# Kernel tuning notes

Hardware: AMD Instinct MI355X
Metric: run time of the kernel (lower is better)

The kernel has to match this reference:

```python
import jax, jax.numpy as jnp
import numpy as np

N_NODES = 50000
N_EDGES = 640000
IN_CH = 128
OUT_CH = 128
HID = 2 * OUT_CH  # 256


def _glorot(key, shape):
    fan_in, fan_out = shape
    lim = np.sqrt(6.0 / (fan_in + fan_out)).astype(np.float32)
    return jax.random.uniform(key, shape, jnp.float32, -lim, lim)


def setup_inputs() -> dict:
    key = jax.random.key(0)
    ks = jax.random.split(key, 8)
    x = jax.random.normal(ks[0], (N_NODES, IN_CH), jnp.float32)
    edge_index = jax.random.randint(ks[1], (2, N_EDGES), 0, N_NODES, jnp.int64)
    # SAGEConv layer 1: lin_l (neighbor branch, with bias), lin_r (root branch, no bias)
    w1_l = _glorot(ks[2], (IN_CH, HID))
    b1_l = jnp.zeros((HID,), jnp.float32)
    w1_r = _glorot(ks[3], (IN_CH, HID))
    # SAGEConv layer 2
    w2_l = _glorot(ks[4], (HID, OUT_CH))
    b2_l = jnp.zeros((OUT_CH,), jnp.float32)
    w2_r = _glorot(ks[5], (HID, OUT_CH))
    return {"x": x, "edge_index": edge_index,
            "w1_l": w1_l, "b1_l": b1_l, "w1_r": w1_r,
            "w2_l": w2_l, "b2_l": b2_l, "w2_r": w2_r}


def _sage_conv(x, src, dst, w_l, b_l, w_r):
    # mean aggregation of source-node features onto destination nodes
    msgs = x[src]                                       # [E, C] gather
    agg = jax.ops.segment_sum(msgs, dst, num_segments=N_NODES)  # [N, C]
    cnt = jax.ops.segment_sum(jnp.ones((src.shape[0],), x.dtype), dst,
                              num_segments=N_NODES)     # [N]
    mean = agg / jnp.maximum(cnt, 1.0)[:, None]
    # out = lin_l(mean_neighbors) + lin_r(x_root)
    return mean @ w_l + b_l + x @ w_r


def reference(x, edge_index, w1_l, b1_l, w1_r, w2_l, b2_l, w2_r):
    src, dst = edge_index[0], edge_index[1]
    h = _sage_conv(x, src, dst, w1_l, b1_l, w1_r)
    h = jax.nn.relu(h)
    return _sage_conv(h, src, dst, w2_l, b2_l, w2_r)
```

## Files before the change

### kernel.cpp

```cpp
#include <hip/hip_runtime.h>

#define N_NODES 50000
#define N_EDGES 640000
#define IN_CH 128
#define OUT_CH 128
#define HID 256
#define M_PAD 50048
#define CAP 64

typedef unsigned int uint;
typedef unsigned short ushort;

__device__ __forceinline__ ushort f2b(float f) {
    uint u = __float_as_uint(f);
    u += 0x7FFFu + ((u >> 16) & 1u);
    return (ushort)(u >> 16);
}
__device__ __forceinline__ float b2f_lo(uint u) { return __uint_as_float(u << 16); }
__device__ __forceinline__ float b2f_hi(uint u) { return __uint_as_float(u & 0xFFFF0000u); }
__device__ __forceinline__ uint packb(float lo, float hi) {
    return (uint)f2b(lo) | ((uint)f2b(hi) << 16);
}

__device__ __forceinline__ void gload_lds16(const ushort* g, ushort* l) {
    __builtin_amdgcn_global_load_lds(
        (const __attribute__((address_space(1))) void*)g,
        (__attribute__((address_space(3))) void*)l, 16, 0, 0);
}

__global__ __launch_bounds__(256) void prep(
    const int* __restrict__ src, const int* __restrict__ dst,
    const float* __restrict__ x, const float* __restrict__ w1l,
    const float* __restrict__ w1r, const float* __restrict__ w2l,
    const float* __restrict__ w2r, int* __restrict__ cnt,
    int* __restrict__ col, ushort* __restrict__ xcat,
    ushort* __restrict__ w1f, ushort* __restrict__ w2f) {
    int b = blockIdx.x;
    if (b < 2500) {
        int e = b * 256 + threadIdx.x;
        int d = dst[e];
        int p = atomicAdd(&cnt[d], 1);
        if (p < CAP) col[d * CAP + p] = src[e];
    } else {
        int id = (b - 2500) * 256 + threadIdx.x;
        if (id < 800000) {
            long long base = (long long)id * 8;
            float4 a = *(const float4*)(x + base);
            float4 c = *(const float4*)(x + base + 4);
            uint4 o;
            o.x = packb(a.x, a.y);
            o.y = packb(a.z, a.w);
            o.z = packb(c.x, c.y);
            o.w = packb(c.z, c.w);
            int row = id >> 4;
            int cc = id & 15;
            ((uint4*)xcat)[(size_t)row * 32 + 16 + cc] = o;
        } else if (id < 865536) {
            int i = id - 800000;
            int n0 = i >> 12, kk = (i >> 9) & 7, lane = (i >> 3) & 63, j = i & 7;
            int n = n0 * 16 + (lane & 15);
            int k = kk * 32 + (lane >> 4) * 8 + j;
            float v = (k < 128) ? w1l[k * 256 + n] : w1r[(k - 128) * 256 + n];
            w1f[i] = f2b(v);
        } else {
            int i = id - 865536;
            int n0 = i >> 12, kk = (i >> 9) & 7, lane = (i >> 3) & 63, j = i & 7;
            int n = n0 * 16 + (lane & 15);
            int k = kk * 32 + (lane >> 4) * 8 + j;
            float v = (n < 128) ? w2l[k * 128 + n] : w2r[k * 128 + (n - 128)];
            w2f[i] = f2b(v);
        }
    }
}

__global__ __launch_bounds__(256) void aggregate_mean1(
    const int* __restrict__ cnt, const int* __restrict__ col,
    ushort* __restrict__ xcat) {
    int t = blockIdx.x * 256 + threadIdx.x;
    int node = t >> 4;
    int q = t & 15;
    if (node >= N_NODES) return;
    int degf = cnt[node];
    int deg = min(degf, CAP);
    const int* cb = col + node * CAP;
    float acc[8] = {0.f, 0.f, 0.f, 0.f, 0.f, 0.f, 0.f, 0.f};
    const uint4* f4 = (const uint4*)xcat;
    int j = 0;
    for (; j + 4 <= deg; j += 4) {
        int4 s4 = *(const int4*)(cb + j);
        uint4 v0 = f4[(size_t)s4.x * 32 + 16 + q];
        uint4 v1 = f4[(size_t)s4.y * 32 + 16 + q];
        uint4 v2 = f4[(size_t)s4.z * 32 + 16 + q];
        uint4 v3 = f4[(size_t)s4.w * 32 + 16 + q];
        acc[0] += b2f_lo(v0.x) + b2f_lo(v1.x) + b2f_lo(v2.x) + b2f_lo(v3.x);
        acc[1] += b2f_hi(v0.x) + b2f_hi(v1.x) + b2f_hi(v2.x) + b2f_hi(v3.x);
        acc[2] += b2f_lo(v0.y) + b2f_lo(v1.y) + b2f_lo(v2.y) + b2f_lo(v3.y);
        acc[3] += b2f_hi(v0.y) + b2f_hi(v1.y) + b2f_hi(v2.y) + b2f_hi(v3.y);
        acc[4] += b2f_lo(v0.z) + b2f_lo(v1.z) + b2f_lo(v2.z) + b2f_lo(v3.z);
        acc[5] += b2f_hi(v0.z) + b2f_hi(v1.z) + b2f_hi(v2.z) + b2f_hi(v3.z);
        acc[6] += b2f_lo(v0.w) + b2f_lo(v1.w) + b2f_lo(v2.w) + b2f_lo(v3.w);
        acc[7] += b2f_hi(v0.w) + b2f_hi(v1.w) + b2f_hi(v2.w) + b2f_hi(v3.w);
    }
    for (; j < deg; ++j) {
        uint4 v = f4[(size_t)cb[j] * 32 + 16 + q];
        acc[0] += b2f_lo(v.x); acc[1] += b2f_hi(v.x);
        acc[2] += b2f_lo(v.y); acc[3] += b2f_hi(v.y);
        acc[4] += b2f_lo(v.z); acc[5] += b2f_hi(v.z);
        acc[6] += b2f_lo(v.w); acc[7] += b2f_hi(v.w);
    }
    float inv = 1.0f / fmaxf((float)degf, 1.0f);
    uint4 o;
    o.x = packb(acc[0] * inv, acc[1] * inv);
    o.y = packb(acc[2] * inv, acc[3] * inv);
    o.z = packb(acc[4] * inv, acc[5] * inv);
    o.w = packb(acc[6] * inv, acc[7] * inv);
    ((uint4*)xcat)[(size_t)node * 32 + q] = o;
}

__global__ __launch_bounds__(256) void combine2(
    const ushort* __restrict__ hw, const int* __restrict__ cnt,
    const int* __restrict__ col, const float* __restrict__ bias,
    float* __restrict__ out) {
    int t = blockIdx.x * 256 + threadIdx.x;
    int node = t >> 4;
    int q = t & 15;
    if (node >= N_NODES) return;
    int degf = cnt[node];
    int deg = min(degf, CAP);
    const int* cb = col + node * CAP;
    float acc[8] = {0.f, 0.f, 0.f, 0.f, 0.f, 0.f, 0.f, 0.f};
    const uint4* f4 = (const uint4*)hw;
    int j = 0;
    for (; j + 4 <= deg; j += 4) {
        int4 s4 = *(const int4*)(cb + j);
        uint4 v0 = f4[(size_t)s4.x * 32 + q];
        uint4 v1 = f4[(size_t)s4.y * 32 + q];
        uint4 v2 = f4[(size_t)s4.z * 32 + q];
        uint4 v3 = f4[(size_t)s4.w * 32 + q];
        acc[0] += b2f_lo(v0.x) + b2f_lo(v1.x) + b2f_lo(v2.x) + b2f_lo(v3.x);
        acc[1] += b2f_hi(v0.x) + b2f_hi(v1.x) + b2f_hi(v2.x) + b2f_hi(v3.x);
        acc[2] += b2f_lo(v0.y) + b2f_lo(v1.y) + b2f_lo(v2.y) + b2f_lo(v3.y);
        acc[3] += b2f_hi(v0.y) + b2f_hi(v1.y) + b2f_hi(v2.y) + b2f_hi(v3.y);
        acc[4] += b2f_lo(v0.z) + b2f_lo(v1.z) + b2f_lo(v2.z) + b2f_lo(v3.z);
        acc[5] += b2f_hi(v0.z) + b2f_hi(v1.z) + b2f_hi(v2.z) + b2f_hi(v3.z);
        acc[6] += b2f_lo(v0.w) + b2f_lo(v1.w) + b2f_lo(v2.w) + b2f_lo(v3.w);
        acc[7] += b2f_hi(v0.w) + b2f_hi(v1.w) + b2f_hi(v2.w) + b2f_hi(v3.w);
    }
    for (; j < deg; ++j) {
        uint4 v = f4[(size_t)cb[j] * 32 + q];
        acc[0] += b2f_lo(v.x); acc[1] += b2f_hi(v.x);
        acc[2] += b2f_lo(v.y); acc[3] += b2f_hi(v.y);
        acc[4] += b2f_lo(v.z); acc[5] += b2f_hi(v.z);
        acc[6] += b2f_lo(v.w); acc[7] += b2f_hi(v.w);
    }
    float inv = 1.0f / fmaxf((float)degf, 1.0f);
    uint4 r = f4[(size_t)node * 32 + 16 + q];
    float4 b0 = *(const float4*)(bias + q * 8);
    float4 b1 = *(const float4*)(bias + q * 8 + 4);
    float4 o0, o1;
    o0.x = acc[0] * inv + b2f_lo(r.x) + b0.x;
    o0.y = acc[1] * inv + b2f_hi(r.x) + b0.y;
    o0.z = acc[2] * inv + b2f_lo(r.y) + b0.z;
    o0.w = acc[3] * inv + b2f_hi(r.y) + b0.w;
    o1.x = acc[4] * inv + b2f_lo(r.z) + b1.x;
    o1.y = acc[5] * inv + b2f_hi(r.z) + b1.y;
    o1.z = acc[6] * inv + b2f_lo(r.w) + b1.z;
    o1.w = acc[7] * inv + b2f_hi(r.w) + b1.w;
    *(float4*)(out + (size_t)node * 128 + q * 8) = o0;
    *(float4*)(out + (size_t)node * 128 + q * 8 + 4) = o1;
}

using bf16x8 = __attribute__((ext_vector_type(8))) short;
using f32x4  = __attribute__((ext_vector_type(4))) float;

__global__ __launch_bounds__(256) void fused_gemm(
    const ushort* __restrict__ A, const ushort* __restrict__ w1f,
    const ushort* __restrict__ w2f, const float* __restrict__ b1,
    ushort* __restrict__ hw) {
    __shared__ alignas(16) ushort tile[64 * 256];

    const int tid = threadIdx.x;
    const int lane = tid & 63;
    const int wave = tid >> 6;
    const int quad = lane >> 4;
    const int l16 = lane & 15;
    const int bm = blockIdx.x * 64;

#pragma unroll
    for (int r = 0; r < 8; ++r) {
        int row = r * 8 + (tid >> 5);
        int c = tid & 31;
        int src = (c & 24) | ((c & 7) ^ (row & 7));
        gload_lds16(A + (size_t)(bm + row) * 256 + src * 8, &tile[row * 256 + c * 8]);
    }

    f32x4 acc[4][4];
#pragma unroll
    for (int rt = 0; rt < 4; ++rt)
#pragma unroll
        for (int ct = 0; ct < 4; ++ct) acc[rt][ct] = (f32x4){0.f, 0.f, 0.f, 0.f};

    const size_t bstep = 64 * 8;
    const ushort* w1b = w1f + (((size_t)(wave * 4) * 8) * 64 + lane) * 8;
    const ushort* w2b = w2f + (((size_t)(wave * 4) * 8) * 64 + lane) * 8;

    bf16x8 bc[4], bn[4];
#pragma unroll
    for (int ct = 0; ct < 4; ++ct)
        bc[ct] = *(const bf16x8*)(w1b + (size_t)ct * 8 * bstep);

    __syncthreads();

#pragma unroll
    for (int kk = 0; kk < 8; ++kk) {
        if (kk < 7) {
#pragma unroll
            for (int ct = 0; ct < 4; ++ct)
                bn[ct] = *(const bf16x8*)(w1b + ((size_t)ct * 8 + kk + 1) * bstep);
        }
        bf16x8 af[4];
#pragma unroll
        for (int rt = 0; rt < 4; ++rt) {
            int row = rt * 16 + l16;
            int c = kk * 4 + quad;
            int slot = (c & 24) | ((c & 7) ^ (row & 7));
            af[rt] = *(const bf16x8*)&tile[row * 256 + slot * 8];
        }
#pragma unroll
        for (int ct = 0; ct < 4; ++ct) {
#pragma unroll
            for (int rt = 0; rt < 4; ++rt)
                acc[rt][ct] = __builtin_amdgcn_mfma_f32_16x16x32_bf16(
                    af[rt], bc[ct], acc[rt][ct], 0, 0, 0);
        }
#pragma unroll
        for (int ct = 0; ct < 4; ++ct) bc[ct] = bn[ct];
    }
    __syncthreads();

#pragma unroll
    for (int ct = 0; ct < 4; ++ct) {
        int colg = wave * 64 + ct * 16 + l16;
        float bv = b1[colg];
        int cc = colg >> 3;
        int off = colg & 7;
#pragma unroll
        for (int rt = 0; rt < 4; ++rt) {
#pragma unroll
            for (int reg = 0; reg < 4; ++reg) {
                int row = rt * 16 + quad * 4 + reg;
                int slot = (cc & 24) | ((cc & 7) ^ (row & 7));
                tile[row * 256 + slot * 8 + off] = f2b(fmaxf(acc[rt][ct][reg] + bv, 0.0f));
            }
        }
    }

#pragma unroll
    for (int rt = 0; rt < 4; ++rt)
#pragma unroll
        for (int ct = 0; ct < 4; ++ct) acc[rt][ct] = (f32x4){0.f, 0.f, 0.f, 0.f};

#pragma unroll
    for (int ct = 0; ct < 4; ++ct)
        bc[ct] = *(const bf16x8*)(w2b + (size_t)ct * 8 * bstep);

    __syncthreads();

#pragma unroll
    for (int kk = 0; kk < 8; ++kk) {
        if (kk < 7) {
#pragma unroll
            for (int ct = 0; ct < 4; ++ct)
                bn[ct] = *(const bf16x8*)(w2b + ((size_t)ct * 8 + kk + 1) * bstep);
        }
        bf16x8 af[4];
#pragma unroll
        for (int rt = 0; rt < 4; ++rt) {
            int row = rt * 16 + l16;
            int c = kk * 4 + quad;
            int slot = (c & 24) | ((c & 7) ^ (row & 7));
            af[rt] = *(const bf16x8*)&tile[row * 256 + slot * 8];
        }
#pragma unroll
        for (int ct = 0; ct < 4; ++ct) {
#pragma unroll
            for (int rt = 0; rt < 4; ++rt)
                acc[rt][ct] = __builtin_amdgcn_mfma_f32_16x16x32_bf16(
                    af[rt], bc[ct], acc[rt][ct], 0, 0, 0);
        }
#pragma unroll
        for (int ct = 0; ct < 4; ++ct) bc[ct] = bn[ct];
    }
    __syncthreads();

#pragma unroll
    for (int ct = 0; ct < 4; ++ct) {
        int colg = wave * 64 + ct * 16 + l16;
        int cc = colg >> 3;
        int off = colg & 7;
#pragma unroll
        for (int rt = 0; rt < 4; ++rt) {
#pragma unroll
            for (int reg = 0; reg < 4; ++reg) {
                int row = rt * 16 + quad * 4 + reg;
                int slot = (cc & 24) | ((cc & 7) ^ (row & 7));
                tile[row * 256 + slot * 8 + off] = f2b(acc[rt][ct][reg]);
            }
        }
    }
    __syncthreads();
#pragma unroll
    for (int r = 0; r < 8; ++r) {
        int row = r * 8 + (tid >> 5);
        int c = tid & 31;
        int slot = (c & 24) | ((c & 7) ^ (row & 7));
        uint4 v = *(const uint4*)&tile[row * 256 + slot * 8];
        *(uint4*)(hw + (size_t)(bm + row) * 256 + c * 8) = v;
    }
}

extern "C" void kernel_launch(void* const* d_in, const int* in_sizes, int n_in,
                              void* d_out, int out_size, void* d_ws, size_t ws_size,
                              hipStream_t stream) {
    const float* x    = (const float*)d_in[0];
    const int*   ei   = (const int*)d_in[1];
    const float* w1_l = (const float*)d_in[2];
    const float* b1_l = (const float*)d_in[3];
    const float* w1_r = (const float*)d_in[4];
    const float* w2_l = (const float*)d_in[5];
    const float* b2_l = (const float*)d_in[6];
    const float* w2_r = (const float*)d_in[7];
    float* out = (float*)d_out;

    const int* src = ei;
    const int* dst = ei + N_EDGES;

    int* cnt = (int*)d_ws;
    int* col = cnt + N_NODES;
    size_t int_bytes = (size_t)(N_NODES + N_NODES * CAP) * 4;
    size_t ofs = (int_bytes + 15) & ~(size_t)15;
    ushort* xcat = (ushort*)((char*)d_ws + ofs);
    ushort* hw   = xcat + (size_t)M_PAD * HID;
    ushort* w1f  = hw + (size_t)M_PAD * HID;
    ushort* w2f  = w1f + HID * HID;

    hipMemsetAsync(cnt, 0, (size_t)N_NODES * sizeof(int), stream);

    prep<<<6137, 256, 0, stream>>>(src, dst, x, w1_l, w1_r, w2_l, w2_r,
                                   cnt, col, xcat, w1f, w2f);

    aggregate_mean1<<<N_NODES * 16 / 256, 256, 0, stream>>>(cnt, col, xcat);
    fused_gemm<<<M_PAD / 64, 256, 0, stream>>>(xcat, w1f, w2f, b1_l, hw);
    combine2<<<N_NODES * 16 / 256, 256, 0, stream>>>(hw, cnt, col, b2_l, out);
}
```

Before: 234.3 us.

## Compress adjacency to 16-bit indices, widen gather unroll, deepen GEMM B prefetch

Neighbor indices in the bucketed adjacency are now stored as 16-bit values, which halves index traffic and footprint. The edge-bucketing work uses four edges per thread with vector loads. The two aggregation kernels unroll the gather loop to 8 neighbors per iteration so more loads are in flight. The fused GEMM double-buffers B fragments two k-steps ahead. This relies on node ids fitting in 16 bits, and 50000 < 65536 holds here.

```diff
diff --git a/kernel.cpp b/kernel.cpp
--- a/kernel.cpp
+++ b/kernel.cpp
@@ -33,16 +33,23 @@
     const float* __restrict__ x, const float* __restrict__ w1l,
     const float* __restrict__ w1r, const float* __restrict__ w2l,
     const float* __restrict__ w2r, int* __restrict__ cnt,
-    int* __restrict__ col, ushort* __restrict__ xcat,
+    ushort* __restrict__ col, ushort* __restrict__ xcat,
     ushort* __restrict__ w1f, ushort* __restrict__ w2f) {
     int b = blockIdx.x;
-    if (b < 2500) {
-        int e = b * 256 + threadIdx.x;
-        int d = dst[e];
-        int p = atomicAdd(&cnt[d], 1);
-        if (p < CAP) col[d * CAP + p] = src[e];
+    if (b < 625) {
+        int base = (b * 256 + threadIdx.x) * 4;
+        int4 d4 = *(const int4*)(dst + base);
+        int4 s4 = *(const int4*)(src + base);
+        int p0 = atomicAdd(&cnt[d4.x], 1);
+        int p1 = atomicAdd(&cnt[d4.y], 1);
+        int p2 = atomicAdd(&cnt[d4.z], 1);
+        int p3 = atomicAdd(&cnt[d4.w], 1);
+        if (p0 < CAP) col[d4.x * CAP + p0] = (ushort)s4.x;
+        if (p1 < CAP) col[d4.y * CAP + p1] = (ushort)s4.y;
+        if (p2 < CAP) col[d4.z * CAP + p2] = (ushort)s4.z;
+        if (p3 < CAP) col[d4.w * CAP + p3] = (ushort)s4.w;
     } else {
-        int id = (b - 2500) * 256 + threadIdx.x;
+        int id = (b - 625) * 256 + threadIdx.x;
         if (id < 800000) {
             long long base = (long long)id * 8;
             float4 a = *(const float4*)(x + base);
@@ -74,7 +81,7 @@
 }
 
 __global__ __launch_bounds__(256) void aggregate_mean1(
-    const int* __restrict__ cnt, const int* __restrict__ col,
+    const int* __restrict__ cnt, const ushort* __restrict__ col,
     ushort* __restrict__ xcat) {
     int t = blockIdx.x * 256 + threadIdx.x;
     int node = t >> 4;
@@ -82,24 +89,40 @@
     if (node >= N_NODES) return;
     int degf = cnt[node];
     int deg = min(degf, CAP);
-    const int* cb = col + node * CAP;
+    const ushort* cb = col + node * CAP;
     float acc[8] = {0.f, 0.f, 0.f, 0.f, 0.f, 0.f, 0.f, 0.f};
     const uint4* f4 = (const uint4*)xcat;
     int j = 0;
-    for (; j + 4 <= deg; j += 4) {
-        int4 s4 = *(const int4*)(cb + j);
-        uint4 v0 = f4[(size_t)s4.x * 32 + 16 + q];
-        uint4 v1 = f4[(size_t)s4.y * 32 + 16 + q];
-        uint4 v2 = f4[(size_t)s4.z * 32 + 16 + q];
-        uint4 v3 = f4[(size_t)s4.w * 32 + 16 + q];
-        acc[0] += b2f_lo(v0.x) + b2f_lo(v1.x) + b2f_lo(v2.x) + b2f_lo(v3.x);
-        acc[1] += b2f_hi(v0.x) + b2f_hi(v1.x) + b2f_hi(v2.x) + b2f_hi(v3.x);
-        acc[2] += b2f_lo(v0.y) + b2f_lo(v1.y) + b2f_lo(v2.y) + b2f_lo(v3.y);
-        acc[3] += b2f_hi(v0.y) + b2f_hi(v1.y) + b2f_hi(v2.y) + b2f_hi(v3.y);
-        acc[4] += b2f_lo(v0.z) + b2f_lo(v1.z) + b2f_lo(v2.z) + b2f_lo(v3.z);
-        acc[5] += b2f_hi(v0.z) + b2f_hi(v1.z) + b2f_hi(v2.z) + b2f_hi(v3.z);
-        acc[6] += b2f_lo(v0.w) + b2f_lo(v1.w) + b2f_lo(v2.w) + b2f_lo(v3.w);
-        acc[7] += b2f_hi(v0.w) + b2f_hi(v1.w) + b2f_hi(v2.w) + b2f_hi(v3.w);
+    for (; j + 8 <= deg; j += 8) {
+        uint4 c4 = *(const uint4*)(cb + j);
+        int s0 = c4.x & 0xFFFF, s1 = c4.x >> 16;
+        int s2 = c4.y & 0xFFFF, s3 = c4.y >> 16;
+        int s4 = c4.z & 0xFFFF, s5 = c4.z >> 16;
+        int s6 = c4.w & 0xFFFF, s7 = c4.w >> 16;
+        uint4 v0 = f4[(size_t)s0 * 32 + 16 + q];
+        uint4 v1 = f4[(size_t)s1 * 32 + 16 + q];
+        uint4 v2 = f4[(size_t)s2 * 32 + 16 + q];
+        uint4 v3 = f4[(size_t)s3 * 32 + 16 + q];
+        uint4 v4 = f4[(size_t)s4 * 32 + 16 + q];
+        uint4 v5 = f4[(size_t)s5 * 32 + 16 + q];
+        uint4 v6 = f4[(size_t)s6 * 32 + 16 + q];
+        uint4 v7 = f4[(size_t)s7 * 32 + 16 + q];
+        acc[0] += b2f_lo(v0.x) + b2f_lo(v1.x) + b2f_lo(v2.x) + b2f_lo(v3.x)
+                + b2f_lo(v4.x) + b2f_lo(v5.x) + b2f_lo(v6.x) + b2f_lo(v7.x);
+        acc[1] += b2f_hi(v0.x) + b2f_hi(v1.x) + b2f_hi(v2.x) + b2f_hi(v3.x)
+                + b2f_hi(v4.x) + b2f_hi(v5.x) + b2f_hi(v6.x) + b2f_hi(v7.x);
+        acc[2] += b2f_lo(v0.y) + b2f_lo(v1.y) + b2f_lo(v2.y) + b2f_lo(v3.y)
+                + b2f_lo(v4.y) + b2f_lo(v5.y) + b2f_lo(v6.y) + b2f_lo(v7.y);
+        acc[3] += b2f_hi(v0.y) + b2f_hi(v1.y) + b2f_hi(v2.y) + b2f_hi(v3.y)
+                + b2f_hi(v4.y) + b2f_hi(v5.y) + b2f_hi(v6.y) + b2f_hi(v7.y);
+        acc[4] += b2f_lo(v0.z) + b2f_lo(v1.z) + b2f_lo(v2.z) + b2f_lo(v3.z)
+                + b2f_lo(v4.z) + b2f_lo(v5.z) + b2f_lo(v6.z) + b2f_lo(v7.z);
+        acc[5] += b2f_hi(v0.z) + b2f_hi(v1.z) + b2f_hi(v2.z) + b2f_hi(v3.z)
+                + b2f_hi(v4.z) + b2f_hi(v5.z) + b2f_hi(v6.z) + b2f_hi(v7.z);
+        acc[6] += b2f_lo(v0.w) + b2f_lo(v1.w) + b2f_lo(v2.w) + b2f_lo(v3.w)
+                + b2f_lo(v4.w) + b2f_lo(v5.w) + b2f_lo(v6.w) + b2f_lo(v7.w);
+        acc[7] += b2f_hi(v0.w) + b2f_hi(v1.w) + b2f_hi(v2.w) + b2f_hi(v3.w)
+                + b2f_hi(v4.w) + b2f_hi(v5.w) + b2f_hi(v6.w) + b2f_hi(v7.w);
     }
     for (; j < deg; ++j) {
         uint4 v = f4[(size_t)cb[j] * 32 + 16 + q];
@@ -119,7 +142,7 @@
 
 __global__ __launch_bounds__(256) void combine2(
     const ushort* __restrict__ hw, const int* __restrict__ cnt,
-    const int* __restrict__ col, const float* __restrict__ bias,
+    const ushort* __restrict__ col, const float* __restrict__ bias,
     float* __restrict__ out) {
     int t = blockIdx.x * 256 + threadIdx.x;
     int node = t >> 4;
@@ -127,24 +150,40 @@
     if (node >= N_NODES) return;
     int degf = cnt[node];
     int deg = min(degf, CAP);
-    const int* cb = col + node * CAP;
+    const ushort* cb = col + node * CAP;
     float acc[8] = {0.f, 0.f, 0.f, 0.f, 0.f, 0.f, 0.f, 0.f};
     const uint4* f4 = (const uint4*)hw;
     int j = 0;
-    for (; j + 4 <= deg; j += 4) {
-        int4 s4 = *(const int4*)(cb + j);
-        uint4 v0 = f4[(size_t)s4.x * 32 + q];
-        uint4 v1 = f4[(size_t)s4.y * 32 + q];
-        uint4 v2 = f4[(size_t)s4.z * 32 + q];
-        uint4 v3 = f4[(size_t)s4.w * 32 + q];
-        acc[0] += b2f_lo(v0.x) + b2f_lo(v1.x) + b2f_lo(v2.x) + b2f_lo(v3.x);
-        acc[1] += b2f_hi(v0.x) + b2f_hi(v1.x) + b2f_hi(v2.x) + b2f_hi(v3.x);
-        acc[2] += b2f_lo(v0.y) + b2f_lo(v1.y) + b2f_lo(v2.y) + b2f_lo(v3.y);
-        acc[3] += b2f_hi(v0.y) + b2f_hi(v1.y) + b2f_hi(v2.y) + b2f_hi(v3.y);
-        acc[4] += b2f_lo(v0.z) + b2f_lo(v1.z) + b2f_lo(v2.z) + b2f_lo(v3.z);
-        acc[5] += b2f_hi(v0.z) + b2f_hi(v1.z) + b2f_hi(v2.z) + b2f_hi(v3.z);
-        acc[6] += b2f_lo(v0.w) + b2f_lo(v1.w) + b2f_lo(v2.w) + b2f_lo(v3.w);
-        acc[7] += b2f_hi(v0.w) + b2f_hi(v1.w) + b2f_hi(v2.w) + b2f_hi(v3.w);
+    for (; j + 8 <= deg; j += 8) {
+        uint4 c4 = *(const uint4*)(cb + j);
+        int s0 = c4.x & 0xFFFF, s1 = c4.x >> 16;
+        int s2 = c4.y & 0xFFFF, s3 = c4.y >> 16;
+        int s4 = c4.z & 0xFFFF, s5 = c4.z >> 16;
+        int s6 = c4.w & 0xFFFF, s7 = c4.w >> 16;
+        uint4 v0 = f4[(size_t)s0 * 32 + q];
+        uint4 v1 = f4[(size_t)s1 * 32 + q];
+        uint4 v2 = f4[(size_t)s2 * 32 + q];
+        uint4 v3 = f4[(size_t)s3 * 32 + q];
+        uint4 v4 = f4[(size_t)s4 * 32 + q];
+        uint4 v5 = f4[(size_t)s5 * 32 + q];
+        uint4 v6 = f4[(size_t)s6 * 32 + q];
+        uint4 v7 = f4[(size_t)s7 * 32 + q];
+        acc[0] += b2f_lo(v0.x) + b2f_lo(v1.x) + b2f_lo(v2.x) + b2f_lo(v3.x)
+                + b2f_lo(v4.x) + b2f_lo(v5.x) + b2f_lo(v6.x) + b2f_lo(v7.x);
+        acc[1] += b2f_hi(v0.x) + b2f_hi(v1.x) + b2f_hi(v2.x) + b2f_hi(v3.x)
+                + b2f_hi(v4.x) + b2f_hi(v5.x) + b2f_hi(v6.x) + b2f_hi(v7.x);
+        acc[2] += b2f_lo(v0.y) + b2f_lo(v1.y) + b2f_lo(v2.y) + b2f_lo(v3.y)
+                + b2f_lo(v4.y) + b2f_lo(v5.y) + b2f_lo(v6.y) + b2f_lo(v7.y);
+        acc[3] += b2f_hi(v0.y) + b2f_hi(v1.y) + b2f_hi(v2.y) + b2f_hi(v3.y)
+                + b2f_hi(v4.y) + b2f_hi(v5.y) + b2f_hi(v6.y) + b2f_hi(v7.y);
+        acc[4] += b2f_lo(v0.z) + b2f_lo(v1.z) + b2f_lo(v2.z) + b2f_lo(v3.z)
+                + b2f_lo(v4.z) + b2f_lo(v5.z) + b2f_lo(v6.z) + b2f_lo(v7.z);
+        acc[5] += b2f_hi(v0.z) + b2f_hi(v1.z) + b2f_hi(v2.z) + b2f_hi(v3.z)
+                + b2f_hi(v4.z) + b2f_hi(v5.z) + b2f_hi(v6.z) + b2f_hi(v7.z);
+        acc[6] += b2f_lo(v0.w) + b2f_lo(v1.w) + b2f_lo(v2.w) + b2f_lo(v3.w)
+                + b2f_lo(v4.w) + b2f_lo(v5.w) + b2f_lo(v6.w) + b2f_lo(v7.w);
+        acc[7] += b2f_hi(v0.w) + b2f_hi(v1.w) + b2f_hi(v2.w) + b2f_hi(v3.w)
+                + b2f_hi(v4.w) + b2f_hi(v5.w) + b2f_hi(v6.w) + b2f_hi(v7.w);
     }
     for (; j < deg; ++j) {
         uint4 v = f4[(size_t)cb[j] * 32 + q];
@@ -204,19 +243,22 @@
     const ushort* w1b = w1f + (((size_t)(wave * 4) * 8) * 64 + lane) * 8;
     const ushort* w2b = w2f + (((size_t)(wave * 4) * 8) * 64 + lane) * 8;
 
-    bf16x8 bc[4], bn[4];
-#pragma unroll
-    for (int ct = 0; ct < 4; ++ct)
-        bc[ct] = *(const bf16x8*)(w1b + (size_t)ct * 8 * bstep);
+    bf16x8 bp[2][4];
+#pragma unroll
+    for (int ct = 0; ct < 4; ++ct) {
+        bp[0][ct] = *(const bf16x8*)(w1b + ((size_t)ct * 8 + 0) * bstep);
+        bp[1][ct] = *(const bf16x8*)(w1b + ((size_t)ct * 8 + 1) * bstep);
+    }
 
     __syncthreads();
 
 #pragma unroll
     for (int kk = 0; kk < 8; ++kk) {
-        if (kk < 7) {
+        bf16x8 bn[4];
+        if (kk < 6) {
 #pragma unroll
             for (int ct = 0; ct < 4; ++ct)
-                bn[ct] = *(const bf16x8*)(w1b + ((size_t)ct * 8 + kk + 1) * bstep);
+                bn[ct] = *(const bf16x8*)(w1b + ((size_t)ct * 8 + kk + 2) * bstep);
         }
         bf16x8 af[4];
 #pragma unroll
@@ -231,12 +273,20 @@
 #pragma unroll
             for (int rt = 0; rt < 4; ++rt)
                 acc[rt][ct] = __builtin_amdgcn_mfma_f32_16x16x32_bf16(
-                    af[rt], bc[ct], acc[rt][ct], 0, 0, 0);
-        }
-#pragma unroll
-        for (int ct = 0; ct < 4; ++ct) bc[ct] = bn[ct];
+                    af[rt], bp[kk & 1][ct], acc[rt][ct], 0, 0, 0);
+        }
+        if (kk < 6) {
+#pragma unroll
+            for (int ct = 0; ct < 4; ++ct) bp[kk & 1][ct] = bn[ct];
+        }
     }
     __syncthreads();
+
+#pragma unroll
+    for (int ct = 0; ct < 4; ++ct) {
+        bp[0][ct] = *(const bf16x8*)(w2b + ((size_t)ct * 8 + 0) * bstep);
+        bp[1][ct] = *(const bf16x8*)(w2b + ((size_t)ct * 8 + 1) * bstep);
+    }
 
 #pragma unroll
     for (int ct = 0; ct < 4; ++ct) {
@@ -260,18 +310,15 @@
 #pragma unroll
         for (int ct = 0; ct < 4; ++ct) acc[rt][ct] = (f32x4){0.f, 0.f, 0.f, 0.f};
 
-#pragma unroll
-    for (int ct = 0; ct < 4; ++ct)
-        bc[ct] = *(const bf16x8*)(w2b + (size_t)ct * 8 * bstep);
-
     __syncthreads();
 
 #pragma unroll
     for (int kk = 0; kk < 8; ++kk) {
-        if (kk < 7) {
+        bf16x8 bn[4];
+        if (kk < 6) {
 #pragma unroll
             for (int ct = 0; ct < 4; ++ct)
-                bn[ct] = *(const bf16x8*)(w2b + ((size_t)ct * 8 + kk + 1) * bstep);
+                bn[ct] = *(const bf16x8*)(w2b + ((size_t)ct * 8 + kk + 2) * bstep);
         }
         bf16x8 af[4];
 #pragma unroll
@@ -286,10 +333,12 @@
 #pragma unroll
             for (int rt = 0; rt < 4; ++rt)
                 acc[rt][ct] = __builtin_amdgcn_mfma_f32_16x16x32_bf16(
-                    af[rt], bc[ct], acc[rt][ct], 0, 0, 0);
-        }
-#pragma unroll
-        for (int ct = 0; ct < 4; ++ct) bc[ct] = bn[ct];
+                    af[rt], bp[kk & 1][ct], acc[rt][ct], 0, 0, 0);
+        }
+        if (kk < 6) {
+#pragma unroll
+            for (int ct = 0; ct < 4; ++ct) bp[kk & 1][ct] = bn[ct];
+        }
     }
     __syncthreads();
 
@@ -336,9 +385,9 @@
     const int* dst = ei + N_EDGES;
 
     int* cnt = (int*)d_ws;
-    int* col = cnt + N_NODES;
-    size_t int_bytes = (size_t)(N_NODES + N_NODES * CAP) * 4;
-    size_t ofs = (int_bytes + 15) & ~(size_t)15;
+    ushort* col = (ushort*)(cnt + N_NODES);
+    size_t ib = (size_t)N_NODES * 4 + (size_t)N_NODES * CAP * 2;
+    size_t ofs = (ib + 15) & ~(size_t)15;
     ushort* xcat = (ushort*)((char*)d_ws + ofs);
     ushort* hw   = xcat + (size_t)M_PAD * HID;
     ushort* w1f  = hw + (size_t)M_PAD * HID;
@@ -346,8 +395,8 @@
 
     hipMemsetAsync(cnt, 0, (size_t)N_NODES * sizeof(int), stream);
 
-    prep<<<6137, 256, 0, stream>>>(src, dst, x, w1_l, w1_r, w2_l, w2_r,
-                                   cnt, col, xcat, w1f, w2f);
+    prep<<<625 + 3637, 256, 0, stream>>>(src, dst, x, w1_l, w1_r, w2_l, w2_r,
+                                         cnt, col, xcat, w1f, w2f);
 
     aggregate_mean1<<<N_NODES * 16 / 256, 256, 0, stream>>>(cnt, col, xcat);
     fused_gemm<<<M_PAD / 64, 256, 0, stream>>>(xcat, w1f, w2f, b1_l, hw);
```

Result: no change. 234.8 us (+0.2%).
